# Kernel tuning notes

Measured on AMD Instinct MI355X. Metric: run time of the kernel, lower is better.

## Reference

```python
import jax, jax.numpy as jnp
import numpy as np

N_USER = 100000
N_ITEM = 100000
E = 500000
EMB, HID, OUT = 128, 128, 64


def _mean_agg(msg_src, src, dst, n_dst):
    """Gather per-edge messages from src nodes, segment-mean onto dst nodes."""
    m = msg_src[src]  # [E, d]
    s = jax.ops.segment_sum(m, dst, num_segments=n_dst)
    cnt = jax.ops.segment_sum(jnp.ones((src.shape[0],), m.dtype), dst,
                              num_segments=n_dst)
    # DGL mean reducer yields 0 for nodes with no in-edges
    return jnp.where(cnt[:, None] > 0, s / jnp.maximum(cnt, 1.0)[:, None], 0.0)


def _layer(feat_u, feat_i, W0, b0, Wui, bui, Wiu, biu,
           src_ui, dst_ui, src_iu, dst_iu):
    # shared self-transform (weight0) -> residual h0 on every ntype
    h0_u = feat_u @ W0 + b0
    h0_i = feat_i @ W0 + b0
    # per-etype transform of source features
    wh_u = feat_u @ Wui + bui  # messages along user->item
    wh_i = feat_i @ Wiu + biu  # messages along item->user
    h_i = _mean_agg(wh_u, src_ui, dst_ui, N_ITEM) + h0_i
    h_u = _mean_agg(wh_i, src_iu, dst_iu, N_USER) + h0_u
    return h_u, h_i


def setup_inputs() -> dict:
    key = jax.random.key(0)
    ks = jax.random.split(key, 12)
    sc_e = 1.0 / np.sqrt(EMB)
    sc_h = 1.0 / np.sqrt(HID)
    return {
        "emb_user": jax.random.normal(ks[0], (N_USER, EMB), jnp.float32),
        "emb_item": jax.random.normal(ks[1], (N_ITEM, EMB), jnp.float32),
        "W1_0": jax.random.normal(ks[2], (EMB, HID), jnp.float32) * sc_e,
        "b1_0": jnp.zeros((HID,), jnp.float32),
        "W1_ui": jax.random.normal(ks[3], (EMB, HID), jnp.float32) * sc_e,
        "b1_ui": jnp.zeros((HID,), jnp.float32),
        "W1_iu": jax.random.normal(ks[4], (EMB, HID), jnp.float32) * sc_e,
        "b1_iu": jnp.zeros((HID,), jnp.float32),
        "W2_0": jax.random.normal(ks[5], (HID, OUT), jnp.float32) * sc_h,
        "b2_0": jnp.zeros((OUT,), jnp.float32),
        "W2_ui": jax.random.normal(ks[6], (HID, OUT), jnp.float32) * sc_h,
        "b2_ui": jnp.zeros((OUT,), jnp.float32),
        "W2_iu": jax.random.normal(ks[7], (HID, OUT), jnp.float32) * sc_h,
        "b2_iu": jnp.zeros((OUT,), jnp.float32),
        "src_ui": jax.random.randint(ks[8], (E,), 0, N_USER, jnp.int32),
        "dst_ui": jax.random.randint(ks[9], (E,), 0, N_ITEM, jnp.int32),
        "src_iu": jax.random.randint(ks[10], (E,), 0, N_ITEM, jnp.int32),
        "dst_iu": jax.random.randint(ks[11], (E,), 0, N_USER, jnp.int32),
    }


def reference(emb_user, emb_item,
              W1_0, b1_0, W1_ui, b1_ui, W1_iu, b1_iu,
              W2_0, b2_0, W2_ui, b2_ui, W2_iu, b2_iu,
              src_ui, dst_ui, src_iu, dst_iu):
    h_u, h_i = _layer(emb_user, emb_item, W1_0, b1_0, W1_ui, b1_ui,
                      W1_iu, b1_iu, src_ui, dst_ui, src_iu, dst_iu)
    h_u = jax.nn.leaky_relu(h_u, 0.01)  # torch F.leaky_relu default slope
    h_i = jax.nn.leaky_relu(h_i, 0.01)
    h_u, h_i = _layer(h_u, h_i, W2_0, b2_0, W2_ui, b2_ui,
                      W2_iu, b2_iu, src_ui, dst_ui, src_iu, dst_iu)
    return h_u, h_i
```

## Files before the change

### kernel.cpp

```cpp
#include <hip/hip_runtime.h>

#define N_USER 100000
#define N_ITEM 100000
#define NEDGE  500000
#define DEGCAP 32

#define B_FILL 978
#define B_CONV 12500
#define B_WT   384
#define B_TOT  (B_FILL + B_CONV + B_WT)

typedef __attribute__((ext_vector_type(8))) short short8;
typedef __attribute__((ext_vector_type(4))) float f32x4;

__device__ __forceinline__ unsigned short f2bf(float f) {
  union { float f; unsigned int u; } x{f};
  unsigned int r = x.u + 0x7fffu + ((x.u >> 16) & 1u);
  return (unsigned short)(r >> 16);
}
__device__ __forceinline__ float bf2f(unsigned short u) {
  union { unsigned int u; float f; } x{(unsigned int)u << 16};
  return x.f;
}

__global__ __launch_bounds__(256) void setup_k(
    const int* __restrict__ src_ui, const int* __restrict__ dst_ui,
    int* __restrict__ cur_i, int* __restrict__ csr_ui,
    const int* __restrict__ src_iu, const int* __restrict__ dst_iu,
    int* __restrict__ cur_u, int* __restrict__ csr_iu,
    const float* __restrict__ emb_u, const float* __restrict__ emb_i,
    unsigned short* __restrict__ ebu, unsigned short* __restrict__ ebi,
    const float* __restrict__ W10, const float* __restrict__ W1ui,
    const float* __restrict__ W1iu, const float* __restrict__ W20,
    const float* __restrict__ W2ui, const float* __restrict__ W2iu,
    unsigned short* __restrict__ WT1i, unsigned short* __restrict__ WT1u,
    unsigned short* __restrict__ WT2i, unsigned short* __restrict__ WT2u) {
  int b = (int)(((unsigned long long)blockIdx.x * 7919ull) % (unsigned long long)B_TOT);
  int tid = threadIdx.x;
  if (b < B_FILL) {
    const int *src, *dst; int *cur, *csr;
    int bb = b;
    if (bb < 489) { src = src_ui; dst = dst_ui; cur = cur_i; csr = csr_ui; }
    else { bb -= 489; src = src_iu; dst = dst_iu; cur = cur_u; csr = csr_iu; }
    int e0 = bb * 1024 + tid;
    int d[4], s[4];
    bool ok[4];
#pragma unroll
    for (int k = 0; k < 4; ++k) {
      int e = e0 + k * 256;
      ok[k] = (e < NEDGE);
      d[k] = ok[k] ? dst[e] : 0;
      s[k] = ok[k] ? src[e] : 0;
    }
    int p[4];
#pragma unroll
    for (int k = 0; k < 4; ++k)
      p[k] = ok[k] ? atomicAdd(&cur[d[k]], 1) : DEGCAP;
#pragma unroll
    for (int k = 0; k < 4; ++k)
      if (ok[k] && p[k] < DEGCAP) csr[d[k] * DEGCAP + p[k]] = s[k];
  } else if (b < B_FILL + B_CONV) {
    int blk = b - B_FILL;
    const float* src; unsigned short* dstp;
    if (blk < 6250) { src = emb_u; dstp = ebu; }
    else { blk -= 6250; src = emb_i; dstp = ebi; }
    size_t g = (size_t)blk * 2048 + (size_t)tid * 8;
    float4 x = *(const float4*)(src + g);
    float4 y = *(const float4*)(src + g + 4);
    short8 v{(short)f2bf(x.x), (short)f2bf(x.y), (short)f2bf(x.z), (short)f2bf(x.w),
             (short)f2bf(y.x), (short)f2bf(y.y), (short)f2bf(y.z), (short)f2bf(y.w)};
    *(short8*)(dstp + g) = v;
  } else {
    int t = (b - B_FILL - B_CONV) * 256 + tid;
    if (t < 32768) {
      int n = t >> 8, k = t & 255;
      float v = (k < 128) ? W10[k * 128 + n] : W1ui[(k - 128) * 128 + n];
      WT1i[t] = f2bf(v);
    } else if (t < 65536) {
      int q = t - 32768; int n = q >> 8, k = q & 255;
      float v = (k < 128) ? W10[k * 128 + n] : W1iu[(k - 128) * 128 + n];
      WT1u[q] = f2bf(v);
    } else if (t < 81920) {
      int q = t - 65536; int n = q >> 8, k = q & 255;
      float v = (k < 128) ? W20[k * 64 + n] : W2ui[(k - 128) * 64 + n];
      WT2i[q] = f2bf(v);
    } else {
      int q = t - 81920; int n = q >> 8, k = q & 255;
      float v = (k < 128) ? W20[k * 64 + n] : W2iu[(k - 128) * 64 + n];
      WT2u[q] = f2bf(v);
    }
  }
}

__global__ __launch_bounds__(256) void aggc_k(
    const unsigned short* __restrict__ featA, const int* __restrict__ curA,
    const int* __restrict__ csrA, unsigned short* __restrict__ outA,
    const unsigned short* __restrict__ featB, const int* __restrict__ curB,
    const int* __restrict__ csrB, unsigned short* __restrict__ outB,
    int nbA) {
  __shared__ int sidx[16][32];
  int b = blockIdx.x;
  const unsigned short* feat; const int* cur; const int* csr; unsigned short* out;
  if (b < nbA) { feat = featA; cur = curA; csr = csrA; out = outA; }
  else { b -= nbA; feat = featB; cur = curB; csr = csrB; out = outB; }
  int grp = threadIdx.x >> 4;
  int ln  = threadIdx.x & 15;
  int node = b * 16 + grp;
  int deg = min(cur[node], DEGCAP);

  int2 sl = *(const int2*)(csr + (size_t)node * DEGCAP + ln * 2);
  sidx[grp][ln * 2] = sl.x;
  sidx[grp][ln * 2 + 1] = sl.y;
  __syncthreads();

  const int* lidx = sidx[grp];
  float a[8] = {0, 0, 0, 0, 0, 0, 0, 0};
  int j = 0;
  if (j + 4 <= deg) {
    int i0 = lidx[0], i1 = lidx[1], i2 = lidx[2], i3 = lidx[3];
    for (;;) {
      bool more = (j + 8 <= deg);
      int n0, n1, n2, n3;
      if (more) { n0 = lidx[j + 4]; n1 = lidx[j + 5]; n2 = lidx[j + 6]; n3 = lidx[j + 7]; }
      short8 v0 = *(const short8*)(feat + (size_t)i0 * 128 + ln * 8);
      short8 v1 = *(const short8*)(feat + (size_t)i1 * 128 + ln * 8);
      short8 v2 = *(const short8*)(feat + (size_t)i2 * 128 + ln * 8);
      short8 v3 = *(const short8*)(feat + (size_t)i3 * 128 + ln * 8);
#pragma unroll
      for (int d = 0; d < 8; ++d)
        a[d] += (bf2f((unsigned short)v0[d]) + bf2f((unsigned short)v1[d])) +
                (bf2f((unsigned short)v2[d]) + bf2f((unsigned short)v3[d]));
      j += 4;
      if (!more) break;
      i0 = n0; i1 = n1; i2 = n2; i3 = n3;
    }
  }
  if (j + 2 <= deg) {
    int i0 = lidx[j], i1 = lidx[j + 1];
    short8 v0 = *(const short8*)(feat + (size_t)i0 * 128 + ln * 8);
    short8 v1 = *(const short8*)(feat + (size_t)i1 * 128 + ln * 8);
#pragma unroll
    for (int d = 0; d < 8; ++d)
      a[d] += bf2f((unsigned short)v0[d]) + bf2f((unsigned short)v1[d]);
    j += 2;
  }
  if (j < deg) {
    short8 v = *(const short8*)(feat + (size_t)lidx[j] * 128 + ln * 8);
#pragma unroll
    for (int d = 0; d < 8; ++d) a[d] += bf2f((unsigned short)v[d]);
  }
  float sc = deg ? 1.f / (float)deg : 0.f;
  short8 pk;
#pragma unroll
  for (int d = 0; d < 8; ++d) pk[d] = (short)f2bf(a[d] * sc);
  *(short8*)(out + (size_t)node * 128 + ln * 8) = pk;
}

template <int N, bool LRELU, bool OUTBF16>
__global__ __launch_bounds__(256) void gemm2_k(
    const unsigned short* __restrict__ A1a, const unsigned short* __restrict__ A2a,
    const unsigned short* __restrict__ WTa, const float* __restrict__ b0a,
    const float* __restrict__ bea, const int* __restrict__ cura,
    void* __restrict__ outa,
    const unsigned short* __restrict__ A1b, const unsigned short* __restrict__ A2b,
    const unsigned short* __restrict__ WTb, const float* __restrict__ b0b,
    const float* __restrict__ beb, const int* __restrict__ curb,
    void* __restrict__ outb, int M, int nbA) {
  constexpr int BM = 64;
  constexpr int CPW = N / 4;
  constexpr int NCF = CPW / 16;
  __shared__ short As[BM * 128];
  __shared__ short Ws[N * 128];
  __shared__ float degmask[BM];

  int blk = blockIdx.x;
  const unsigned short* A1; const unsigned short* A2; const unsigned short* WT;
  const float* b0; const float* be; const int* cur; void* outv;
  if (blk < nbA) { A1 = A1a; A2 = A2a; WT = WTa; b0 = b0a; be = bea; cur = cura; outv = outa; }
  else { blk -= nbA; A1 = A1b; A2 = A2b; WT = WTb; b0 = b0b; be = beb; cur = curb; outv = outb; }

  const int tid = threadIdx.x;
  const int lane = tid & 63;
  const int wave = tid >> 6;
  const int row0 = blk * BM;
  const int colbase = wave * CPW;

  if (tid < BM) {
    int r = row0 + tid;
    degmask[tid] = (r < M && cur[r] > 0) ? 1.f : 0.f;
  }

  f32x4 acc[4][NCF] = {};

#pragma unroll
  for (int kh = 0; kh < 2; ++kh) {
    __syncthreads();
    const unsigned short* base = (kh == 0) ? A1 : A2;
#pragma unroll
    for (int it = 0; it < 4; ++it) {
      int chunk = tid + it * 256;
      int row = chunk >> 4, c16 = chunk & 15;
      int gr = row0 + row; if (gr > M - 1) gr = M - 1;
      short8 v = *(const short8*)(base + (size_t)gr * 128 + c16 * 8);
      int byteoff = row * 256 + ((c16 * 16) ^ ((row & 7) << 4));
      *(short8*)((char*)As + byteoff) = v;
    }
#pragma unroll
    for (int it = 0; it < (N * 16) / 256; ++it) {
      int chunk = tid + it * 256;
      int n = chunk >> 4, c16 = chunk & 15;
      short8 v = *(const short8*)(WT + (size_t)n * 256 + kh * 128 + c16 * 8);
      int byteoff = n * 256 + ((c16 * 16) ^ ((n & 7) << 4));
      *(short8*)((char*)Ws + byteoff) = v;
    }
    __syncthreads();

#pragma unroll
    for (int ks = 0; ks < 4; ++ks) {
      short8 af[4];
#pragma unroll
      for (int rf = 0; rf < 4; ++rf) {
        int row = rf * 16 + (lane & 15);
        int c16 = ks * 4 + (lane >> 4);
        int byteoff = row * 256 + ((c16 * 16) ^ ((row & 7) << 4));
        af[rf] = *(const short8*)((const char*)As + byteoff);
      }
      short8 wf[NCF];
#pragma unroll
      for (int cf = 0; cf < NCF; ++cf) {
        int n = colbase + cf * 16 + (lane & 15);
        int c16 = ks * 4 + (lane >> 4);
        int byteoff = n * 256 + ((c16 * 16) ^ ((n & 7) << 4));
        wf[cf] = *(const short8*)((const char*)Ws + byteoff);
      }
#pragma unroll
      for (int rf = 0; rf < 4; ++rf)
#pragma unroll
        for (int cf = 0; cf < NCF; ++cf)
          acc[rf][cf] = __builtin_amdgcn_mfma_f32_16x16x32_bf16(
              af[rf], wf[cf], acc[rf][cf], 0, 0, 0);
    }
  }

#pragma unroll
  for (int cf = 0; cf < NCF; ++cf) {
    int c = colbase + cf * 16 + (lane & 15);
    float bb0 = b0[c], bbe = be[c];
#pragma unroll
    for (int rf = 0; rf < 4; ++rf) {
#pragma unroll
      for (int j = 0; j < 4; ++j) {
        int lr = rf * 16 + (lane >> 4) * 4 + j;
        int r = row0 + lr;
        if (r < M) {
          float v = acc[rf][cf][j] + bb0 + degmask[lr] * bbe;
          if (LRELU) v = (v >= 0.f) ? v : 0.01f * v;
          if (OUTBF16)
            ((unsigned short*)outv)[(size_t)r * N + c] = f2bf(v);
          else
            ((float*)outv)[(size_t)r * N + c] = v;
        }
      }
    }
  }
}

extern "C" void kernel_launch(void* const* d_in, const int* in_sizes, int n_in,
                              void* d_out, int out_size, void* d_ws,
                              size_t ws_size, hipStream_t stream) {
  const float* emb_u = (const float*)d_in[0];
  const float* emb_i = (const float*)d_in[1];
  const float* W1_0  = (const float*)d_in[2];
  const float* b1_0  = (const float*)d_in[3];
  const float* W1_ui = (const float*)d_in[4];
  const float* b1_ui = (const float*)d_in[5];
  const float* W1_iu = (const float*)d_in[6];
  const float* b1_iu = (const float*)d_in[7];
  const float* W2_0  = (const float*)d_in[8];
  const float* b2_0  = (const float*)d_in[9];
  const float* W2_ui = (const float*)d_in[10];
  const float* b2_ui = (const float*)d_in[11];
  const float* W2_iu = (const float*)d_in[12];
  const float* b2_iu = (const float*)d_in[13];
  const int* src_ui = (const int*)d_in[14];
  const int* dst_ui = (const int*)d_in[15];
  const int* src_iu = (const int*)d_in[16];
  const int* dst_iu = (const int*)d_in[17];
  float* out = (float*)d_out;

  char* p = (char*)d_ws;
  unsigned short* WT1i = (unsigned short*)p; p += 65536;
  unsigned short* WT1u = (unsigned short*)p; p += 65536;
  unsigned short* WT2i = (unsigned short*)p; p += 32768;
  unsigned short* WT2u = (unsigned short*)p; p += 32768;
  int* cur_i = (int*)p; p += 400128;
  int* cur_u = (int*)p; p += 400128;
  int* csr_ui = (int*)p; p += (size_t)100032 * DEGCAP * 4;
  int* csr_iu = (int*)p; p += (size_t)100032 * DEGCAP * 4;
  const size_t FB = (size_t)N_USER * 128 * 2;
  unsigned short* ebu  = (unsigned short*)p; p += FB;
  unsigned short* ebi  = (unsigned short*)p; p += FB;
  unsigned short* hu = ebu;
  unsigned short* hi = ebi;
  unsigned short* aggB = (unsigned short*)out;
  unsigned short* aggA = (unsigned short*)(out + (size_t)N_USER * 64);

  const int GG = (N_USER + 63) / 64;

  hipMemsetAsync(cur_i, 0, 2 * 400128, stream);
  setup_k<<<B_TOT, 256, 0, stream>>>(src_ui, dst_ui, cur_i, csr_ui,
                                     src_iu, dst_iu, cur_u, csr_iu,
                                     emb_u, emb_i, ebu, ebi,
                                     W1_0, W1_ui, W1_iu, W2_0, W2_ui, W2_iu,
                                     WT1i, WT1u, WT2i, WT2u);

  aggc_k<<<2 * 6250, 256, 0, stream>>>(
      ebu, cur_i, csr_ui, aggA, ebi, cur_u, csr_iu, aggB, 6250);
  gemm2_k<128, true, true><<<2 * GG, 256, 0, stream>>>(
      ebi, aggA, WT1i, b1_0, b1_ui, cur_i, hi,
      ebu, aggB, WT1u, b1_0, b1_iu, cur_u, hu, N_USER, GG);

  aggc_k<<<2 * 6250, 256, 0, stream>>>(
      hu, cur_i, csr_ui, aggA, hi, cur_u, csr_iu, aggB, 6250);
  gemm2_k<64, false, false><<<2 * GG, 256, 0, stream>>>(
      hi, aggA, WT2i, b2_0, b2_ui, cur_i, out + (size_t)N_USER * 64,
      hu, aggB, WT2u, b2_0, b2_iu, cur_u, out, N_USER, GG);
}
```

Measured before the change: 229.3 us.

## Partition CSR fill by destination range to localize atomics across XCDs

The CSR fill phase of the setup kernel is restructured. Each of eight partitions, selected by blockIdx & 7, scans a chunk of edges and handles only edges whose destination falls in its node range, with fill blocks spaced every seventh block among the conversion blocks. The apparent intent is that blocks mapped to the same XCD touch disjoint counter and CSR regions, so atomics and writes stay in a local L2. The cost is that every edge index is read eight times and each fill block runs a longer serial loop.

```diff
diff --git a/kernel.cpp b/kernel.cpp
--- a/kernel.cpp
+++ b/kernel.cpp
@@ -4,11 +4,10 @@
 #define N_ITEM 100000
 #define NEDGE  500000
 #define DEGCAP 32
-
-#define B_FILL 978
-#define B_CONV 12500
-#define B_WT   384
-#define B_TOT  (B_FILL + B_CONV + B_WT)
+#define NPART  12504
+
+#define B_FILLN 976
+#define B_TOT   13860
 
 typedef __attribute__((ext_vector_type(8))) short short8;
 typedef __attribute__((ext_vector_type(4))) float f32x4;
@@ -35,59 +34,58 @@
     const float* __restrict__ W2ui, const float* __restrict__ W2iu,
     unsigned short* __restrict__ WT1i, unsigned short* __restrict__ WT1u,
     unsigned short* __restrict__ WT2i, unsigned short* __restrict__ WT2u) {
-  int b = (int)(((unsigned long long)blockIdx.x * 7919ull) % (unsigned long long)B_TOT);
-  int tid = threadIdx.x;
-  if (b < B_FILL) {
-    const int *src, *dst; int *cur, *csr;
-    int bb = b;
-    if (bb < 489) { src = src_ui; dst = dst_ui; cur = cur_i; csr = csr_ui; }
-    else { bb -= 489; src = src_iu; dst = dst_iu; cur = cur_u; csr = csr_iu; }
-    int e0 = bb * 1024 + tid;
-    int d[4], s[4];
-    bool ok[4];
-#pragma unroll
-    for (int k = 0; k < 4; ++k) {
-      int e = e0 + k * 256;
-      ok[k] = (e < NEDGE);
-      d[k] = ok[k] ? dst[e] : 0;
-      s[k] = ok[k] ? src[e] : 0;
-    }
-    int p[4];
-#pragma unroll
-    for (int k = 0; k < 4; ++k)
-      p[k] = ok[k] ? atomicAdd(&cur[d[k]], 1) : DEGCAP;
-#pragma unroll
-    for (int k = 0; k < 4; ++k)
-      if (ok[k] && p[k] < DEGCAP) csr[d[k] * DEGCAP + p[k]] = s[k];
-  } else if (b < B_FILL + B_CONV) {
-    int blk = b - B_FILL;
-    const float* src; unsigned short* dstp;
-    if (blk < 6250) { src = emb_u; dstp = ebu; }
-    else { blk -= 6250; src = emb_i; dstp = ebi; }
-    size_t g = (size_t)blk * 2048 + (size_t)tid * 8;
-    float4 x = *(const float4*)(src + g);
-    float4 y = *(const float4*)(src + g + 4);
-    short8 v{(short)f2bf(x.x), (short)f2bf(x.y), (short)f2bf(x.z), (short)f2bf(x.w),
-             (short)f2bf(y.x), (short)f2bf(y.y), (short)f2bf(y.z), (short)f2bf(y.w)};
-    *(short8*)(dstp + g) = v;
+  int r = blockIdx.x, tid = threadIdx.x;
+  bool isfill = (r % 7 == 0) && (r / 7 < B_FILLN);
+  if (isfill) {
+    int fi = r / 7;
+    int p = r & 7;
+    int rank = fi >> 3;
+    int lo = p * NPART, hi = lo + NPART;
+    int e0 = rank * 8197;
+    int e1 = e0 + 8197; if (e1 > 2 * NEDGE) e1 = 2 * NEDGE;
+    for (int e = e0 + tid; e < e1; e += 256) {
+      const int *src, *dst; int *cur, *csr; int ee = e;
+      if (ee < NEDGE) { src = src_ui; dst = dst_ui; cur = cur_i; csr = csr_ui; }
+      else { ee -= NEDGE; src = src_iu; dst = dst_iu; cur = cur_u; csr = csr_iu; }
+      int d = dst[ee];
+      if (d >= lo && d < hi) {
+        int pos = atomicAdd(&cur[d], 1);
+        if (pos < DEGCAP) csr[d * DEGCAP + pos] = src[ee];
+      }
+    }
   } else {
-    int t = (b - B_FILL - B_CONV) * 256 + tid;
-    if (t < 32768) {
-      int n = t >> 8, k = t & 255;
-      float v = (k < 128) ? W10[k * 128 + n] : W1ui[(k - 128) * 128 + n];
-      WT1i[t] = f2bf(v);
-    } else if (t < 65536) {
-      int q = t - 32768; int n = q >> 8, k = q & 255;
-      float v = (k < 128) ? W10[k * 128 + n] : W1iu[(k - 128) * 128 + n];
-      WT1u[q] = f2bf(v);
-    } else if (t < 81920) {
-      int q = t - 65536; int n = q >> 8, k = q & 255;
-      float v = (k < 128) ? W20[k * 64 + n] : W2ui[(k - 128) * 64 + n];
-      WT2i[q] = f2bf(v);
+    int nf = (r + 6) / 7; if (nf > B_FILLN) nf = B_FILLN;
+    int sr = r - nf;
+    if (sr < 12500) {
+      int blk = sr;
+      const float* src; unsigned short* dstp;
+      if (blk < 6250) { src = emb_u; dstp = ebu; }
+      else { blk -= 6250; src = emb_i; dstp = ebi; }
+      size_t g = (size_t)blk * 2048 + (size_t)tid * 8;
+      float4 x = *(const float4*)(src + g);
+      float4 y = *(const float4*)(src + g + 4);
+      short8 v{(short)f2bf(x.x), (short)f2bf(x.y), (short)f2bf(x.z), (short)f2bf(x.w),
+               (short)f2bf(y.x), (short)f2bf(y.y), (short)f2bf(y.z), (short)f2bf(y.w)};
+      *(short8*)(dstp + g) = v;
     } else {
-      int q = t - 81920; int n = q >> 8, k = q & 255;
-      float v = (k < 128) ? W20[k * 64 + n] : W2iu[(k - 128) * 64 + n];
-      WT2u[q] = f2bf(v);
+      int t = (sr - 12500) * 256 + tid;
+      if (t < 32768) {
+        int n = t >> 8, k = t & 255;
+        float v = (k < 128) ? W10[k * 128 + n] : W1ui[(k - 128) * 128 + n];
+        WT1i[t] = f2bf(v);
+      } else if (t < 65536) {
+        int q = t - 32768; int n = q >> 8, k = q & 255;
+        float v = (k < 128) ? W10[k * 128 + n] : W1iu[(k - 128) * 128 + n];
+        WT1u[q] = f2bf(v);
+      } else if (t < 81920) {
+        int q = t - 65536; int n = q >> 8, k = q & 255;
+        float v = (k < 128) ? W20[k * 64 + n] : W2ui[(k - 128) * 64 + n];
+        WT2i[q] = f2bf(v);
+      } else {
+        int q = t - 81920; int n = q >> 8, k = q & 255;
+        float v = (k < 128) ? W20[k * 64 + n] : W2iu[(k - 128) * 64 + n];
+        WT2u[q] = f2bf(v);
+      }
     }
   }
 }
```

Result: slower. 237.5 us (+3.6%).

## Merge CSR fill blocks across edge types and prefetch both A halves into registers

Applied to the files above, without the earlier changes.

The setup kernel's CSR-fill section now uses 256 blocks, each looping over 4096 edges that span both edge types. The hashed block-index scrambling that interleaved work types is removed, so blocks run in plain order. The GEMM kernel now loads both K-halves of the A tile (A1 and A2) into registers up front, so the second half's global load is issued early instead of after the first half's compute. This costs extra registers and could lower occupancy, and fewer fill blocks means less parallelism for the atomics.

```diff
diff --git a/kernel.cpp b/kernel.cpp
--- a/kernel.cpp
+++ b/kernel.cpp
@@ -5,7 +5,7 @@
 #define NEDGE  500000
 #define DEGCAP 32
 
-#define B_FILL 978
+#define B_FILL 256
 #define B_CONV 12500
 #define B_WT   384
 #define B_TOT  (B_FILL + B_CONV + B_WT)
@@ -35,30 +35,36 @@
     const float* __restrict__ W2ui, const float* __restrict__ W2iu,
     unsigned short* __restrict__ WT1i, unsigned short* __restrict__ WT1u,
     unsigned short* __restrict__ WT2i, unsigned short* __restrict__ WT2u) {
-  int b = (int)(((unsigned long long)blockIdx.x * 7919ull) % (unsigned long long)B_TOT);
-  int tid = threadIdx.x;
+  int b = blockIdx.x, tid = threadIdx.x;
   if (b < B_FILL) {
-    const int *src, *dst; int *cur, *csr;
-    int bb = b;
-    if (bb < 489) { src = src_ui; dst = dst_ui; cur = cur_i; csr = csr_ui; }
-    else { bb -= 489; src = src_iu; dst = dst_iu; cur = cur_u; csr = csr_iu; }
-    int e0 = bb * 1024 + tid;
-    int d[4], s[4];
-    bool ok[4];
-#pragma unroll
-    for (int k = 0; k < 4; ++k) {
-      int e = e0 + k * 256;
-      ok[k] = (e < NEDGE);
-      d[k] = ok[k] ? dst[e] : 0;
-      s[k] = ok[k] ? src[e] : 0;
-    }
-    int p[4];
-#pragma unroll
-    for (int k = 0; k < 4; ++k)
-      p[k] = ok[k] ? atomicAdd(&cur[d[k]], 1) : DEGCAP;
-#pragma unroll
-    for (int k = 0; k < 4; ++k)
-      if (ok[k] && p[k] < DEGCAP) csr[d[k] * DEGCAP + p[k]] = s[k];
+    int chunk = b * 4096;
+#pragma unroll 1
+    for (int it = 0; it < 4; ++it) {
+      int e0 = chunk + it * 1024 + tid;
+      int d[4], s[4];
+      int* curp[4]; int* csrp[4];
+      bool ok[4];
+#pragma unroll
+      for (int k = 0; k < 4; ++k) {
+        int e = e0 + k * 256;
+        ok[k] = (e < 2 * NEDGE);
+        bool g0 = (e < NEDGE);
+        int ee = g0 ? e : e - NEDGE;
+        const int* dp = g0 ? dst_ui : dst_iu;
+        const int* sp = g0 ? src_ui : src_iu;
+        curp[k] = g0 ? cur_i : cur_u;
+        csrp[k] = g0 ? csr_ui : csr_iu;
+        d[k] = ok[k] ? dp[ee] : 0;
+        s[k] = ok[k] ? sp[ee] : 0;
+      }
+      int p[4];
+#pragma unroll
+      for (int k = 0; k < 4; ++k)
+        p[k] = ok[k] ? atomicAdd(&curp[k][d[k]], 1) : DEGCAP;
+#pragma unroll
+      for (int k = 0; k < 4; ++k)
+        if (ok[k] && p[k] < DEGCAP) csrp[k][d[k] * DEGCAP + p[k]] = s[k];
+    }
   } else if (b < B_FILL + B_CONV) {
     int blk = b - B_FILL;
     const float* src; unsigned short* dstp;
@@ -185,6 +191,16 @@
   const int row0 = blk * BM;
   const int colbase = wave * CPW;
 
+  short8 aA[4], aB[4];
+#pragma unroll
+  for (int it = 0; it < 4; ++it) {
+    int chunk = tid + it * 256;
+    int row = chunk >> 4, c16 = chunk & 15;
+    int gr = row0 + row; if (gr > M - 1) gr = M - 1;
+    aA[it] = *(const short8*)(A1 + (size_t)gr * 128 + c16 * 8);
+    aB[it] = *(const short8*)(A2 + (size_t)gr * 128 + c16 * 8);
+  }
+
   if (tid < BM) {
     int r = row0 + tid;
     degmask[tid] = (r < M && cur[r] > 0) ? 1.f : 0.f;
@@ -195,15 +211,12 @@
 #pragma unroll
   for (int kh = 0; kh < 2; ++kh) {
     __syncthreads();
-    const unsigned short* base = (kh == 0) ? A1 : A2;
 #pragma unroll
     for (int it = 0; it < 4; ++it) {
       int chunk = tid + it * 256;
       int row = chunk >> 4, c16 = chunk & 15;
-      int gr = row0 + row; if (gr > M - 1) gr = M - 1;
-      short8 v = *(const short8*)(base + (size_t)gr * 128 + c16 * 8);
       int byteoff = row * 256 + ((c16 * 16) ^ ((row & 7) << 4));
-      *(short8*)((char*)As + byteoff) = v;
+      *(short8*)((char*)As + byteoff) = (kh == 0) ? aA[it] : aB[it];
     }
 #pragma unroll
     for (int it = 0; it < (N * 16) / 256; ++it) {
```

After: 225.9 us. No clear change (-1.5%).
